# Kernel tuning notes

Measured on AMD Instinct MI355X. Metric: run time of the kernel, lower is better.

## Reference

```python
import jax, jax.numpy as jnp
import numpy as np

ROPE_BASE = 10000.0


def _apply_rope(x, positions):
    # x: [B, S, H, Dh], positions: [S]
    d_head = x.shape[-1]
    half = d_head // 2
    inv_freq = 1.0 / (ROPE_BASE ** (jnp.arange(0, half, dtype=jnp.float32) * 2.0 / d_head))
    angles = positions.astype(jnp.float32)[:, None] * inv_freq[None, :]  # [S, half]
    cos = jnp.cos(angles)[None, :, None, :]  # [1,S,1,half]
    sin = jnp.sin(angles)[None, :, None, :]
    x1, x2 = jnp.split(x, 2, axis=-1)
    return jnp.concatenate([x1 * cos - x2 * sin, x1 * sin + x2 * cos], axis=-1)


def _alibi_slopes(n_heads):
    # standard ALiBi slopes: 2^(-8*(h+1)/n_heads)
    return 2.0 ** (-8.0 * (jnp.arange(1, n_heads + 1, dtype=jnp.float32) / n_heads))


def setup_inputs() -> dict:
    key = jax.random.key(0)
    ks = jax.random.split(key, 5)
    B, S, D = 2, 2048, 2048
    H, KVH, Dh = 16, 4, 128
    std = 0.02
    return {
        "residual": jax.random.normal(ks[0], (B, S, D), dtype=jnp.float32),
        "W_Q": jax.random.normal(ks[1], (H, Dh, D), dtype=jnp.float32) * std,
        "W_K": jax.random.normal(ks[2], (KVH, Dh, D), dtype=jnp.float32) * std,
        "W_V": jax.random.normal(ks[3], (KVH, Dh, D), dtype=jnp.float32) * std,
        "W_O": jax.random.normal(ks[4], (H, Dh, D), dtype=jnp.float32) * std,
        "start_pos": 0,
    }


def reference(residual, W_Q, W_K, W_V, W_O, start_pos):
    B, S, D = residual.shape
    H, Dh, _ = W_Q.shape
    KVH = W_K.shape[0]
    # projections (prefill path: cache=None, total_len == S)
    q = jnp.einsum('bsd,hed->bshe', residual, W_Q)   # [B,S,H,Dh]
    k = jnp.einsum('bsd,hed->bshe', residual, W_K)   # [B,S,KVH,Dh]
    v = jnp.einsum('bsd,hed->bshe', residual, W_V)   # [B,S,KVH,Dh]
    # RoPE
    positions = start_pos + jnp.arange(S)
    q = _apply_rope(q, positions)
    k = _apply_rope(k, positions)
    k_for_cache = k
    v_for_cache = v
    # GQA head repeat
    rep = H // KVH
    k_r = jnp.repeat(k, rep, axis=2)
    v_r = jnp.repeat(v, rep, axis=2)
    # attention scores [B,H,Sq,Sk]
    scores = jnp.einsum('bqhe,bkhe->bhqk', q, k_r) / jnp.sqrt(jnp.float32(Dh))
    # ALiBi bias (sliced rows start_pos:start_pos+S of the total_len x total_len bias)
    slopes = _alibi_slopes(H)  # [H]
    qpos = start_pos + jnp.arange(S)
    kpos = jnp.arange(S)
    bias = -slopes[:, None, None] * (qpos[:, None] - kpos[None, :]).astype(jnp.float32)
    scores = scores + bias[None, :, :, :]
    # causal mask: keep j <= i (tril of ones)
    mask = kpos[None, :] <= qpos[:, None]  # with start_pos=0 this is tril
    scores = jnp.where(mask[None, None, :, :], scores, -jnp.inf)
    pattern = jax.nn.softmax(scores, axis=-1)
    attn = jnp.einsum('bhqk,bkhe->bqhe', pattern, v_r)
    output = jnp.einsum('bqhe,hed->bqd', attn, W_O)
    return output, k_for_cache, v_for_cache
```

## Files before the change

kernel.cpp:

```cpp
#include <hip/hip_runtime.h>


typedef __attribute__((ext_vector_type(8))) short frag8;
typedef __attribute__((ext_vector_type(4))) float facc4;

#define DEVI __device__ __forceinline__

constexpr int Bc  = 2;
constexpr int Sc  = 2048;
constexpr int Dc  = 2048;
constexpr int Hc  = 16;
constexpr int KVHc = 4;
constexpr int Dhc = 128;
constexpr int Mc  = Bc * Sc;
constexpr int NQc = Hc * Dhc;
constexpr int NKVc = KVHc * Dhc;

DEVI unsigned short f2bf(float f) {
  union { float f; unsigned u; } v; v.f = f;
  return (unsigned short)((v.u + 0x7fffu + ((v.u >> 16) & 1u)) >> 16);
}
DEVI float bf2f(unsigned short h) {
  union { unsigned u; float f; } v; v.u = ((unsigned)h) << 16;
  return v.f;
}

DEVI void gload_lds16(const void* g, void* l) {
  __builtin_amdgcn_global_load_lds(
      (const __attribute__((address_space(1))) unsigned int*)g,
      (__attribute__((address_space(3))) unsigned int*)l, 16, 0, 0);
}

DEVI float rowred_max(float x) {
  union { float f; int i; } a, b;
  a.f = x;
  b.i = __builtin_amdgcn_update_dpp(a.i, a.i, 0x128, 0xF, 0xF, false); a.f = fmaxf(a.f, b.f);
  b.i = __builtin_amdgcn_update_dpp(a.i, a.i, 0x124, 0xF, 0xF, false); a.f = fmaxf(a.f, b.f);
  b.i = __builtin_amdgcn_update_dpp(a.i, a.i, 0x122, 0xF, 0xF, false); a.f = fmaxf(a.f, b.f);
  b.i = __builtin_amdgcn_update_dpp(a.i, a.i, 0x121, 0xF, 0xF, false); a.f = fmaxf(a.f, b.f);
  return a.f;
}
DEVI float rowred_sum(float x) {
  union { float f; int i; } a, b;
  a.f = x;
  b.i = __builtin_amdgcn_update_dpp(a.i, a.i, 0x128, 0xF, 0xF, false); a.f += b.f;
  b.i = __builtin_amdgcn_update_dpp(a.i, a.i, 0x124, 0xF, 0xF, false); a.f += b.f;
  b.i = __builtin_amdgcn_update_dpp(a.i, a.i, 0x122, 0xF, 0xF, false); a.f += b.f;
  b.i = __builtin_amdgcn_update_dpp(a.i, a.i, 0x121, 0xF, 0xF, false); a.f += b.f;
  return a.f;
}


__global__ void cvt_f32_bf16(const float* __restrict__ in,
                             unsigned short* __restrict__ out, int n) {
  int i = (blockIdx.x * 256 + threadIdx.x) * 4;
  if (i < n) {
    float4 v = *(const float4*)(in + i);
    ushort4 o;
    o.x = f2bf(v.x); o.y = f2bf(v.y); o.z = f2bf(v.z); o.w = f2bf(v.w);
    *(ushort4*)(out + i) = o;
  }
}

__global__ void cvt_transpose_wo(const float* __restrict__ in,
                                 unsigned short* __restrict__ out) {
  __shared__ float tile[64][65];
  int r0 = blockIdx.y * 64;
  int c0 = blockIdx.x * 64;
  int t = threadIdx.x;
#pragma unroll
  for (int i = 0; i < 16; ++i) {
    int idx = i * 256 + t; int r = idx >> 6, c = idx & 63;
    tile[r][c] = in[(size_t)(r0 + r) * Dc + c0 + c];
  }
  __syncthreads();
#pragma unroll
  for (int i = 0; i < 16; ++i) {
    int idx = i * 256 + t; int r = idx >> 6, c = idx & 63;
    out[(size_t)(c0 + r) * NQc + r0 + c] = f2bf(tile[c][r]);
  }
}


template <int MODE>
__global__ __launch_bounds__(256) void gemm_nt(
    const unsigned short* __restrict__ Amat,
    const unsigned short* __restrict__ Bmat,
    float* __restrict__ Cf, float* __restrict__ Cf2,
    unsigned short* __restrict__ Cb,
    int Nn, int Kk) {
  __shared__ __align__(16) unsigned short As[128 * 32];
  __shared__ __align__(16) unsigned short Bs[128 * 32];
  int t = threadIdx.x;
  int lane = t & 63, w = t >> 6;
  int quad = lane >> 4, l16 = lane & 15;
  int wm = (w >> 1) * 64, wn = (w & 1) * 64;
  int m0 = blockIdx.x * 128, n0 = blockIdx.y * 128;

  facc4 acc[4][4] = {};

  const int nIter = Kk / 32;
  for (int kt = 0; kt < nIter; ++kt) {
    __syncthreads();
#pragma unroll
    for (int i = 0; i < 2; ++i) {
      int c = i * 256 + t;
      int row = c >> 2, ch = c & 3;
      gload_lds16(Amat + (size_t)(m0 + row) * Kk + kt * 32 + ch * 8, &As[c * 8]);
      gload_lds16(Bmat + (size_t)(n0 + row) * Kk + kt * 32 + ch * 8, &Bs[c * 8]);
    }
    asm volatile("s_waitcnt vmcnt(0)" ::: "memory");
    __syncthreads();

    frag8 aF[4], bF[4];
#pragma unroll
    for (int mi = 0; mi < 4; ++mi)
      aF[mi] = *(const frag8*)&As[(wm + mi * 16 + l16) * 32 + quad * 8];
#pragma unroll
    for (int ni = 0; ni < 4; ++ni)
      bF[ni] = *(const frag8*)&Bs[(wn + ni * 16 + l16) * 32 + quad * 8];
#pragma unroll
    for (int mi = 0; mi < 4; ++mi)
#pragma unroll
      for (int ni = 0; ni < 4; ++ni)
        acc[mi][ni] = __builtin_amdgcn_mfma_f32_16x16x32_bf16(
            aF[mi], bF[ni], acc[mi][ni], 0, 0, 0);
  }

#pragma unroll
  for (int mi = 0; mi < 4; ++mi)
#pragma unroll
    for (int ni = 0; ni < 4; ++ni)
#pragma unroll
      for (int i = 0; i < 4; ++i) {
        int mrow = m0 + wm + mi * 16 + quad * 4 + i;
        int ncol = n0 + wn + ni * 16 + l16;
        float v = acc[mi][ni][i];
        if (MODE == 0) {
          Cf[(size_t)mrow * Nn + ncol] = v;
        } else if (MODE == 1) {
          Cb[(size_t)mrow * Nn + ncol] = f2bf(v);
        } else {
          if (ncol < NKVc) {
            Cf[(size_t)mrow * NKVc + ncol] = v;
          } else {
            int nc = ncol - NKVc;
            Cf2[(size_t)mrow * NKVc + nc] = v;
            int b = mrow >> 11, s = mrow & (Sc - 1);
            Cb[((size_t)(b * NKVc + nc)) * Sc + s] = f2bf(v);
          }
        }
      }
}


__global__ void rope_q(unsigned short* qb, const int* __restrict__ sp) {
  int idx = blockIdx.x * 256 + threadIdx.x;
  int e = idx & 63, h = (idx >> 6) & 15, m = idx >> 10;
  int s = m & (Sc - 1);
  float pos = (float)(sp[0] + s);
  float invf = exp2f(-(float)e * 0.20762050593046835f);
  float ang = pos * invf;
  float sn, cs; sincosf(ang, &sn, &cs);
  size_t base = (size_t)m * NQc + h * Dhc + e;
  float x1 = bf2f(qb[base]), x2 = bf2f(qb[base + 64]);
  qb[base]      = f2bf(x1 * cs - x2 * sn);
  qb[base + 64] = f2bf(x1 * sn + x2 * cs);
}

__global__ void rope_k(float* kf, unsigned short* kb, const int* __restrict__ sp) {
  int idx = blockIdx.x * 256 + threadIdx.x;
  int e = idx & 63, kvh = (idx >> 6) & 3, m = idx >> 8;
  int s = m & (Sc - 1);
  float pos = (float)(sp[0] + s);
  float invf = exp2f(-(float)e * 0.20762050593046835f);
  float ang = pos * invf;
  float sn, cs; sincosf(ang, &sn, &cs);
  size_t base = (size_t)m * NKVc + kvh * Dhc + e;
  float x1 = kf[base], x2 = kf[base + 64];
  float o1 = x1 * cs - x2 * sn;
  float o2 = x1 * sn + x2 * cs;
  kf[base] = o1; kf[base + 64] = o2;
  kb[base] = f2bf(o1); kb[base + 64] = f2bf(o2);
}


DEVI void issue_tile(const unsigned short* kb, const unsigned short* vbT,
                     int bb, int kvh, int kt, int t,
                     unsigned short* KsB, unsigned short* VtB) {
#pragma unroll
  for (int i = 0; i < 4; ++i) {
    int c = i * 256 + t;
    int row = c >> 4, chp = c & 15;
    int ch = chp ^ (row & 15);
    gload_lds16(kb + (size_t)(bb * Sc + kt * 64 + row) * NKVc + kvh * Dhc + ch * 8,
                KsB + c * 8);
  }
#pragma unroll
  for (int i = 0; i < 4; ++i) {
    int c = i * 256 + t;
    int row = c >> 3, chp = c & 7;
    int ch = chp ^ (row & 7);
    gload_lds16(vbT + ((size_t)(bb * KVHc + kvh) * Dhc + row) * Sc + kt * 64 + ch * 8,
                VtB + c * 8);
  }
}

DEVI void load_q(frag8 (&aQc)[4], const unsigned short* qb, int bb, int qt,
                 int h, int w, int quad, int l16) {
  const unsigned short* qrow =
      qb + (size_t)(bb * Sc + qt * 64 + w * 16 + l16) * NQc + h * Dhc;
#pragma unroll
  for (int kd = 0; kd < 4; ++kd)
    aQc[kd] = *(const frag8*)(qrow + (kd * 4 + quad) * 8);
}

DEVI void write_o(unsigned short* qb, facc4 (&oacc)[8], float (&lrow)[4],
                  int bb, int qt, int h, int w, int quad, int l16) {
  float rinv[4];
#pragma unroll
  for (int i = 0; i < 4; ++i) rinv[i] = 1.0f / rowred_sum(lrow[i]);
#pragma unroll
  for (int c8 = 0; c8 < 8; ++c8)
#pragma unroll
    for (int i = 0; i < 4; ++i) {
      int row = qt * 64 + w * 16 + quad * 4 + i;
      size_t o = ((size_t)(bb * Sc + row) * Hc + h) * Dhc + c8 * 16 + l16;
      qb[o] = f2bf(oacc[c8][i] * rinv[i]);
    }
}

__global__ __launch_bounds__(256, 2) void flash_attn(
    unsigned short* qb,
    const unsigned short* __restrict__ kb,
    const unsigned short* __restrict__ vbT,
    const int* __restrict__ spp) {
  __shared__ __align__(16) unsigned short Ks[2][64 * 128];
  __shared__ __align__(16) unsigned short Vt[2][128 * 64];
  __shared__ __align__(16) unsigned short Ps[4][16 * 64];

  int g = blockIdx.x & 7;
  int bb = g >> 2, kvh = g & 3;
  int inner = blockIdx.x >> 3;
  int pair = inner & 15, hh = inner >> 4;
  int h = kvh * 4 + hh;
  int qtA = pair, qtB = 31 - pair;

  int t = threadIdx.x, lane = t & 63, w = t >> 6;
  int quad = lane >> 4, l16 = lane & 15;
  int sp = spp[0];
  constexpr float LOG2E = 1.4426950408889634f;
  const float SC = 0.08838834764831845f * LOG2E;
  const float THR = 8.0f;
  float slope2 = exp2f(-0.5f * (float)(h + 1)) * LOG2E;

  int tA = min((sp + qtA * 64 + 63) >> 6, 31) + 1;
  int tB = min((sp + qtB * 64 + 63) >> 6, 31) + 1;
  int total = tA + tB;

  frag8 aQc[4];
  load_q(aQc, qb, bb, qtA, h, w, quad, l16);

  facc4 oacc[8] = {};
  float mrow[4], lrow[4];
  int qposi[4]; float bq[4];
  int qt = qtA;
#pragma unroll
  for (int i = 0; i < 4; ++i) {
    mrow[i] = -1e30f; lrow[i] = 0.f;
    qposi[i] = sp + qt * 64 + w * 16 + quad * 4 + i;
    bq[i] = slope2 * (float)qposi[i];
  }

  issue_tile(kb, vbT, bb, kvh, tA - 1, t, Ks[0], Vt[0]);

  for (int it = 0; it < total; ++it) {
    if (it == tA) {
      write_o(qb, oacc, lrow, bb, qtA, h, w, quad, l16);
      load_q(aQc, qb, bb, qtB, h, w, quad, l16);
      qt = qtB;
#pragma unroll
      for (int c8 = 0; c8 < 8; ++c8)
#pragma unroll
        for (int i = 0; i < 4; ++i) oacc[c8][i] = 0.f;
#pragma unroll
      for (int i = 0; i < 4; ++i) {
        mrow[i] = -1e30f; lrow[i] = 0.f;
        qposi[i] = sp + qt * 64 + w * 16 + quad * 4 + i;
        bq[i] = slope2 * (float)qposi[i];
      }
    }
    int kt = (it < tA) ? (tA - 1 - it) : (total - 1 - it);

    if (it + 1 < total) {
      int nk = (it + 1 < tA) ? (tA - 2 - it) : (total - 2 - it);
      issue_tile(kb, vbT, bb, kvh, nk, t, Ks[(it + 1) & 1], Vt[(it + 1) & 1]);
      asm volatile("s_waitcnt vmcnt(8)" ::: "memory");
    } else {
      asm volatile("s_waitcnt vmcnt(0)" ::: "memory");
    }
    __builtin_amdgcn_s_barrier();
    asm volatile("" ::: "memory");

    const unsigned short* KsB = Ks[it & 1];
    const unsigned short* VtB = Vt[it & 1];

    facc4 sacc[4] = {};
#pragma unroll
    for (int kd = 0; kd < 4; ++kd) {
      int ch = kd * 4 + quad;
#pragma unroll
      for (int c4 = 0; c4 < 4; ++c4) {
        frag8 bK = *(const frag8*)&KsB[(c4 * 16 + l16) * 128 + (ch ^ l16) * 8];
        sacc[c4] = __builtin_amdgcn_mfma_f32_16x16x32_bf16(aQc[kd], bK, sacc[c4], 0, 0, 0);
      }
    }

    bool needmask = (kt * 64 + 63) > (sp + qt * 64);
    float sv[4][4];
    float mt[4] = {-1e30f, -1e30f, -1e30f, -1e30f};
    float bk0 = slope2 * (float)(kt * 64 + l16);
    float s2x16 = slope2 * 16.0f;
#pragma unroll
    for (int c4 = 0; c4 < 4; ++c4) {
      float bk = bk0 + (float)c4 * s2x16;
      int kpos = kt * 64 + c4 * 16 + l16;
#pragma unroll
      for (int i = 0; i < 4; ++i) {
        float v = fmaf(sacc[c4][i], SC, bk - bq[i]);
        if (needmask) v = (kpos <= qposi[i]) ? v : -1e30f;
        sv[c4][i] = v;
        mt[i] = fmaxf(mt[i], v);
      }
    }

    int need = (mt[0] > mrow[0] + THR) || (mt[1] > mrow[1] + THR) ||
               (mt[2] > mrow[2] + THR) || (mt[3] > mrow[3] + THR);
    if (__any(need)) {
      float alpha[4];
#pragma unroll
      for (int i = 0; i < 4; ++i) mt[i] = rowred_max(mt[i]);
#pragma unroll
      for (int i = 0; i < 4; ++i) {
        float mn = fmaxf(mrow[i], mt[i]);
        alpha[i] = exp2f(mrow[i] - mn);
        mrow[i] = mn;
        lrow[i] *= alpha[i];
      }
#pragma unroll
      for (int c8 = 0; c8 < 8; ++c8)
#pragma unroll
        for (int i = 0; i < 4; ++i) oacc[c8][i] *= alpha[i];
    }

#pragma unroll
    for (int c4 = 0; c4 < 4; ++c4) {
      float p0 = exp2f(sv[c4][0] - mrow[0]);
      float p1 = exp2f(sv[c4][1] - mrow[1]);
      float p2 = exp2f(sv[c4][2] - mrow[2]);
      float p3 = exp2f(sv[c4][3] - mrow[3]);
      lrow[0] += p0; lrow[1] += p1; lrow[2] += p2; lrow[3] += p3;
      unsigned u01, u23;
      asm("v_cvt_pk_bf16_f32 %0, %1, %2" : "=v"(u01) : "v"(p0), "v"(p1));
      asm("v_cvt_pk_bf16_f32 %0, %1, %2" : "=v"(u23) : "v"(p2), "v"(p3));
      int kk = c4 * 16 + l16;
      int col = kk & 7, chnk = kk >> 3;
      int r0 = quad * 4;
      unsigned short* Pw = &Ps[w][0];
      Pw[(r0 + 0) * 64 + ((chnk ^ ((r0 + 0) & 7)) * 8) + col] = (unsigned short)(u01 & 0xffffu);
      Pw[(r0 + 1) * 64 + ((chnk ^ ((r0 + 1) & 7)) * 8) + col] = (unsigned short)(u01 >> 16);
      Pw[(r0 + 2) * 64 + ((chnk ^ ((r0 + 2) & 7)) * 8) + col] = (unsigned short)(u23 & 0xffffu);
      Pw[(r0 + 3) * 64 + ((chnk ^ ((r0 + 3) & 7)) * 8) + col] = (unsigned short)(u23 >> 16);
    }

#pragma unroll
    for (int k2 = 0; k2 < 2; ++k2) {
      int ch = k2 * 4 + quad;
      frag8 aP = *(const frag8*)&Ps[w][l16 * 64 + (ch ^ (l16 & 7)) * 8];
#pragma unroll
      for (int c8 = 0; c8 < 8; ++c8) {
        frag8 bV = *(const frag8*)&VtB[(c8 * 16 + l16) * 64 + (ch ^ (l16 & 7)) * 8];
        oacc[c8] = __builtin_amdgcn_mfma_f32_16x16x32_bf16(aP, bV, oacc[c8], 0, 0, 0);
      }
    }

    asm volatile("" ::: "memory");
    __builtin_amdgcn_s_barrier();
  }

  write_o(qb, oacc, lrow, bb, qtB, h, w, quad, l16);
}


extern "C" void kernel_launch(void* const* d_in, const int* in_sizes, int n_in,
                              void* d_out, int out_size, void* d_ws, size_t ws_size,
                              hipStream_t stream) {
  const float* residual = (const float*)d_in[0];
  const float* W_Q = (const float*)d_in[1];
  const float* W_K = (const float*)d_in[2];
  const float* W_V = (const float*)d_in[3];
  const float* W_O = (const float*)d_in[4];
  const int* start_pos = (const int*)d_in[5];

  float* out = (float*)d_out;
  float* kf = out + (size_t)Bc * Sc * Dc;
  float* vf = kf + (size_t)Mc * NKVc;

  char* w = (char*)d_ws;
  auto alloc = [&](size_t bytes) {
    char* p = w; w += (bytes + 255) & ~(size_t)255; return p;
  };
  unsigned short* rb   = (unsigned short*)alloc((size_t)Mc * Dc * 2);
  unsigned short* wqb  = (unsigned short*)alloc((size_t)NQc * Dc * 2);
  unsigned short* wkvb = (unsigned short*)alloc((size_t)2 * NKVc * Dc * 2);
  unsigned short* wob  = (unsigned short*)alloc((size_t)Dc * NQc * 2);
  unsigned short* qb   = (unsigned short*)alloc((size_t)Mc * NQc * 2);
  unsigned short* kb   = (unsigned short*)alloc((size_t)Mc * NKVc * 2);
  unsigned short* vbT  = (unsigned short*)alloc((size_t)Mc * NKVc * 2);
  (void)ws_size; (void)in_sizes; (void)n_in; (void)out_size;

  cvt_f32_bf16<<<(Mc * Dc) / 1024, 256, 0, stream>>>(residual, rb, Mc * Dc);
  cvt_f32_bf16<<<(NQc * Dc) / 1024, 256, 0, stream>>>(W_Q, wqb, NQc * Dc);
  cvt_f32_bf16<<<(NKVc * Dc) / 1024, 256, 0, stream>>>(W_K, wkvb, NKVc * Dc);
  cvt_f32_bf16<<<(NKVc * Dc) / 1024, 256, 0, stream>>>(W_V, wkvb + (size_t)NKVc * Dc, NKVc * Dc);
  cvt_transpose_wo<<<dim3(32, 32), 256, 0, stream>>>(W_O, wob);

  gemm_nt<1><<<dim3(32, 16), 256, 0, stream>>>(rb, wqb, nullptr, nullptr, qb, NQc, Dc);
  gemm_nt<2><<<dim3(32, 8), 256, 0, stream>>>(rb, wkvb, kf, vf, vbT, 2 * NKVc, Dc);

  rope_q<<<(Mc * Hc * 64) / 256, 256, 0, stream>>>(qb, start_pos);
  rope_k<<<(Mc * KVHc * 64) / 256, 256, 0, stream>>>(kf, kb, start_pos);

  flash_attn<<<512, 256, 0, stream>>>(qb, kb, vbT, start_pos);

  gemm_nt<0><<<dim3(32, 16), 256, 0, stream>>>(qb, wob, out, nullptr, nullptr, Dc, Dc);
}
```

Baseline: 376.6 us.

## Drop running-max tracking in unmasked attention tiles and merge small launches

In flash attention, tiles that are neither the first nor the diagonal tile skip the max reduction and rescaling. They compute exp2 of one FMA, using a precomputed per-column additive offset that shrinks by slope*64 per tile. This works because the ALiBi bias falls as the key tile moves further back. A rare overflow check rescales l, O and the offset by 2^-32 when the row sum grows too large. The conversion kernels and the two RoPE kernels are also merged into single launches to cut launch overhead. The risk is numerical: if scores in far tiles exceed the first tile's max, the exponent could grow, which the overflow guard only partly handles.

```diff
diff --git a/kernel.cpp b/kernel.cpp
--- a/kernel.cpp
+++ b/kernel.cpp
@@ -51,33 +51,44 @@
 }
 
 
-__global__ void cvt_f32_bf16(const float* __restrict__ in,
-                             unsigned short* __restrict__ out, int n) {
-  int i = (blockIdx.x * 256 + threadIdx.x) * 4;
-  if (i < n) {
-    float4 v = *(const float4*)(in + i);
+__global__ void cvt_all(const float* __restrict__ residual,
+                        const float* __restrict__ WQ,
+                        const float* __restrict__ WK,
+                        const float* __restrict__ WV,
+                        const float* __restrict__ WO,
+                        unsigned short* __restrict__ rb,
+                        unsigned short* __restrict__ wqb,
+                        unsigned short* __restrict__ wkvb,
+                        unsigned short* __restrict__ wob) {
+  __shared__ float tile[64][65];
+  int bid = blockIdx.x;
+  int t = threadIdx.x;
+  if (bid < 14336) {
+    const float* src; unsigned short* dst; int off;
+    if (bid < 8192)       { src = residual; dst = rb;  off = bid; }
+    else if (bid < 12288) { src = WQ; dst = wqb; off = bid - 8192; }
+    else if (bid < 13312) { src = WK; dst = wkvb; off = bid - 12288; }
+    else                  { src = WV; dst = wkvb + (size_t)NKVc * Dc; off = bid - 13312; }
+    int i = (off * 256 + t) * 4;
+    float4 v = *(const float4*)(src + i);
     ushort4 o;
     o.x = f2bf(v.x); o.y = f2bf(v.y); o.z = f2bf(v.z); o.w = f2bf(v.w);
-    *(ushort4*)(out + i) = o;
-  }
-}
-
-__global__ void cvt_transpose_wo(const float* __restrict__ in,
-                                 unsigned short* __restrict__ out) {
-  __shared__ float tile[64][65];
-  int r0 = blockIdx.y * 64;
-  int c0 = blockIdx.x * 64;
-  int t = threadIdx.x;
-#pragma unroll
-  for (int i = 0; i < 16; ++i) {
-    int idx = i * 256 + t; int r = idx >> 6, c = idx & 63;
-    tile[r][c] = in[(size_t)(r0 + r) * Dc + c0 + c];
-  }
-  __syncthreads();
-#pragma unroll
-  for (int i = 0; i < 16; ++i) {
-    int idx = i * 256 + t; int r = idx >> 6, c = idx & 63;
-    out[(size_t)(c0 + r) * NQc + r0 + c] = f2bf(tile[c][r]);
+    *(ushort4*)(dst + i) = o;
+  } else {
+    int tb = bid - 14336;
+    int r0 = (tb >> 5) * 64;
+    int c0 = (tb & 31) * 64;
+#pragma unroll
+    for (int i = 0; i < 16; ++i) {
+      int idx = i * 256 + t; int r = idx >> 6, c = idx & 63;
+      tile[r][c] = WO[(size_t)(r0 + r) * Dc + c0 + c];
+    }
+    __syncthreads();
+#pragma unroll
+    for (int i = 0; i < 16; ++i) {
+      int idx = i * 256 + t; int r = idx >> 6, c = idx & 63;
+      wob[(size_t)(c0 + r) * NQc + r0 + c] = f2bf(tile[c][r]);
+    }
   }
 }
 
@@ -154,34 +165,36 @@
 }
 
 
-__global__ void rope_q(unsigned short* qb, const int* __restrict__ sp) {
+__global__ void rope_all(unsigned short* qb, float* kf, unsigned short* kb,
+                         const int* __restrict__ sp) {
   int idx = blockIdx.x * 256 + threadIdx.x;
-  int e = idx & 63, h = (idx >> 6) & 15, m = idx >> 10;
-  int s = m & (Sc - 1);
-  float pos = (float)(sp[0] + s);
-  float invf = exp2f(-(float)e * 0.20762050593046835f);
-  float ang = pos * invf;
-  float sn, cs; sincosf(ang, &sn, &cs);
-  size_t base = (size_t)m * NQc + h * Dhc + e;
-  float x1 = bf2f(qb[base]), x2 = bf2f(qb[base + 64]);
-  qb[base]      = f2bf(x1 * cs - x2 * sn);
-  qb[base + 64] = f2bf(x1 * sn + x2 * cs);
-}
-
-__global__ void rope_k(float* kf, unsigned short* kb, const int* __restrict__ sp) {
-  int idx = blockIdx.x * 256 + threadIdx.x;
-  int e = idx & 63, kvh = (idx >> 6) & 3, m = idx >> 8;
-  int s = m & (Sc - 1);
-  float pos = (float)(sp[0] + s);
-  float invf = exp2f(-(float)e * 0.20762050593046835f);
-  float ang = pos * invf;
-  float sn, cs; sincosf(ang, &sn, &cs);
-  size_t base = (size_t)m * NKVc + kvh * Dhc + e;
-  float x1 = kf[base], x2 = kf[base + 64];
-  float o1 = x1 * cs - x2 * sn;
-  float o2 = x1 * sn + x2 * cs;
-  kf[base] = o1; kf[base + 64] = o2;
-  kb[base] = f2bf(o1); kb[base + 64] = f2bf(o2);
+  constexpr int NQ = Mc * Hc * 64;
+  if (idx < NQ) {
+    int e = idx & 63, h = (idx >> 6) & 15, m = idx >> 10;
+    int s = m & (Sc - 1);
+    float pos = (float)(sp[0] + s);
+    float invf = exp2f(-(float)e * 0.20762050593046835f);
+    float ang = pos * invf;
+    float sn, cs; sincosf(ang, &sn, &cs);
+    size_t base = (size_t)m * NQc + h * Dhc + e;
+    float x1 = bf2f(qb[base]), x2 = bf2f(qb[base + 64]);
+    qb[base]      = f2bf(x1 * cs - x2 * sn);
+    qb[base + 64] = f2bf(x1 * sn + x2 * cs);
+  } else {
+    int j = idx - NQ;
+    int e = j & 63, kvh = (j >> 6) & 3, m = j >> 8;
+    int s = m & (Sc - 1);
+    float pos = (float)(sp[0] + s);
+    float invf = exp2f(-(float)e * 0.20762050593046835f);
+    float ang = pos * invf;
+    float sn, cs; sincosf(ang, &sn, &cs);
+    size_t base = (size_t)m * NKVc + kvh * Dhc + e;
+    float x1 = kf[base], x2 = kf[base + 64];
+    float o1 = x1 * cs - x2 * sn;
+    float o2 = x1 * sn + x2 * cs;
+    kf[base] = o1; kf[base + 64] = o2;
+    kb[base] = f2bf(o1); kb[base + 64] = f2bf(o2);
+  }
 }
 
 
@@ -251,8 +264,9 @@
   int sp = spp[0];
   constexpr float LOG2E = 1.4426950408889634f;
   const float SC = 0.08838834764831845f * LOG2E;
-  const float THR = 8.0f;
   float slope2 = exp2f(-0.5f * (float)(h + 1)) * LOG2E;
+  float s2x16 = slope2 * 16.0f;
+  float s2x64 = slope2 * 64.0f;
 
   int tA = min((sp + qtA * 64 + 63) >> 6, 31) + 1;
   int tB = min((sp + qtB * 64 + 63) >> 6, 31) + 1;
@@ -262,8 +276,8 @@
   load_q(aQc, qb, bb, qtA, h, w, quad, l16);
 
   facc4 oacc[8] = {};
-  float mrow[4], lrow[4];
-  int qposi[4]; float bq[4];
+  float mrow[4], lrow[4], bq[4], adn[4][4];
+  int qposi[4];
   int qt = qtA;
 #pragma unroll
   for (int i = 0; i < 4; ++i) {
@@ -291,6 +305,7 @@
       }
     }
     int kt = (it < tA) ? (tA - 1 - it) : (total - 1 - it);
+    bool first = (it == 0) || (it == tA);
 
     if (it + 1 < total) {
       int nk = (it + 1 < tA) ? (tA - 2 - it) : (total - 2 - it);
@@ -316,61 +331,80 @@
       }
     }
 
+    unsigned short* Pw = &Ps[w][0];
+    int r0 = quad * 4;
     bool needmask = (kt * 64 + 63) > (sp + qt * 64);
-    float sv[4][4];
-    float mt[4] = {-1e30f, -1e30f, -1e30f, -1e30f};
-    float bk0 = slope2 * (float)(kt * 64 + l16);
-    float s2x16 = slope2 * 16.0f;
-#pragma unroll
-    for (int c4 = 0; c4 < 4; ++c4) {
-      float bk = bk0 + (float)c4 * s2x16;
-      int kpos = kt * 64 + c4 * 16 + l16;
-#pragma unroll
-      for (int i = 0; i < 4; ++i) {
-        float v = fmaf(sacc[c4][i], SC, bk - bq[i]);
-        if (needmask) v = (kpos <= qposi[i]) ? v : -1e30f;
-        sv[c4][i] = v;
-        mt[i] = fmaxf(mt[i], v);
-      }
-    }
-
-    int need = (mt[0] > mrow[0] + THR) || (mt[1] > mrow[1] + THR) ||
-               (mt[2] > mrow[2] + THR) || (mt[3] > mrow[3] + THR);
-    if (__any(need)) {
-      float alpha[4];
+
+    if (first || needmask) {
+      float sv[4][4];
+      float mt[4] = {-1e30f, -1e30f, -1e30f, -1e30f};
+#pragma unroll
+      for (int c4 = 0; c4 < 4; ++c4) {
+        int kpos = kt * 64 + c4 * 16 + l16;
+        float bk = slope2 * (float)kpos;
+#pragma unroll
+        for (int i = 0; i < 4; ++i) {
+          float v = fmaf(sacc[c4][i], SC, bk - bq[i]);
+          if (needmask) v = (kpos <= qposi[i]) ? v : -1e30f;
+          sv[c4][i] = v;
+          mt[i] = fmaxf(mt[i], v);
+        }
+      }
 #pragma unroll
       for (int i = 0; i < 4; ++i) mt[i] = rowred_max(mt[i]);
 #pragma unroll
       for (int i = 0; i < 4; ++i) {
         float mn = fmaxf(mrow[i], mt[i]);
-        alpha[i] = exp2f(mrow[i] - mn);
+        float alpha = exp2f(mrow[i] - mn);
         mrow[i] = mn;
-        lrow[i] *= alpha[i];
-      }
-#pragma unroll
-      for (int c8 = 0; c8 < 8; ++c8)
-#pragma unroll
-        for (int i = 0; i < 4; ++i) oacc[c8][i] *= alpha[i];
-    }
-
-#pragma unroll
-    for (int c4 = 0; c4 < 4; ++c4) {
-      float p0 = exp2f(sv[c4][0] - mrow[0]);
-      float p1 = exp2f(sv[c4][1] - mrow[1]);
-      float p2 = exp2f(sv[c4][2] - mrow[2]);
-      float p3 = exp2f(sv[c4][3] - mrow[3]);
-      lrow[0] += p0; lrow[1] += p1; lrow[2] += p2; lrow[3] += p3;
-      unsigned u01, u23;
-      asm("v_cvt_pk_bf16_f32 %0, %1, %2" : "=v"(u01) : "v"(p0), "v"(p1));
-      asm("v_cvt_pk_bf16_f32 %0, %1, %2" : "=v"(u23) : "v"(p2), "v"(p3));
-      int kk = c4 * 16 + l16;
-      int col = kk & 7, chnk = kk >> 3;
-      int r0 = quad * 4;
-      unsigned short* Pw = &Ps[w][0];
-      Pw[(r0 + 0) * 64 + ((chnk ^ ((r0 + 0) & 7)) * 8) + col] = (unsigned short)(u01 & 0xffffu);
-      Pw[(r0 + 1) * 64 + ((chnk ^ ((r0 + 1) & 7)) * 8) + col] = (unsigned short)(u01 >> 16);
-      Pw[(r0 + 2) * 64 + ((chnk ^ ((r0 + 2) & 7)) * 8) + col] = (unsigned short)(u23 & 0xffffu);
-      Pw[(r0 + 3) * 64 + ((chnk ^ ((r0 + 3) & 7)) * 8) + col] = (unsigned short)(u23 >> 16);
+        lrow[i] *= alpha;
+#pragma unroll
+        for (int c8 = 0; c8 < 8; ++c8) oacc[c8][i] *= alpha;
+      }
+#pragma unroll
+      for (int c4 = 0; c4 < 4; ++c4) {
+        float p0 = exp2f(sv[c4][0] - mrow[0]);
+        float p1 = exp2f(sv[c4][1] - mrow[1]);
+        float p2 = exp2f(sv[c4][2] - mrow[2]);
+        float p3 = exp2f(sv[c4][3] - mrow[3]);
+        lrow[0] += p0; lrow[1] += p1; lrow[2] += p2; lrow[3] += p3;
+        unsigned u01, u23;
+        asm("v_cvt_pk_bf16_f32 %0, %1, %2" : "=v"(u01) : "v"(p0), "v"(p1));
+        asm("v_cvt_pk_bf16_f32 %0, %1, %2" : "=v"(u23) : "v"(p2), "v"(p3));
+        int kk = c4 * 16 + l16;
+        int col = kk & 7, chnk = kk >> 3;
+        Pw[(r0 + 0) * 64 + ((chnk ^ ((r0 + 0) & 7)) * 8) + col] = (unsigned short)(u01 & 0xffffu);
+        Pw[(r0 + 1) * 64 + ((chnk ^ ((r0 + 1) & 7)) * 8) + col] = (unsigned short)(u01 >> 16);
+        Pw[(r0 + 2) * 64 + ((chnk ^ ((r0 + 2) & 7)) * 8) + col] = (unsigned short)(u23 & 0xffffu);
+        Pw[(r0 + 3) * 64 + ((chnk ^ ((r0 + 3) & 7)) * 8) + col] = (unsigned short)(u23 >> 16);
+      }
+      float bkn0 = slope2 * (float)((kt - 1) * 64 + l16);
+#pragma unroll
+      for (int c4 = 0; c4 < 4; ++c4) {
+        float bkc = bkn0 + (float)c4 * s2x16;
+#pragma unroll
+        for (int i = 0; i < 4; ++i) adn[c4][i] = bkc - bq[i] - mrow[i];
+      }
+    } else {
+#pragma unroll
+      for (int c4 = 0; c4 < 4; ++c4) {
+        float p0 = exp2f(fmaf(sacc[c4][0], SC, adn[c4][0]));
+        float p1 = exp2f(fmaf(sacc[c4][1], SC, adn[c4][1]));
+        float p2 = exp2f(fmaf(sacc[c4][2], SC, adn[c4][2]));
+        float p3 = exp2f(fmaf(sacc[c4][3], SC, adn[c4][3]));
+        lrow[0] += p0; lrow[1] += p1; lrow[2] += p2; lrow[3] += p3;
+        adn[c4][0] -= s2x64; adn[c4][1] -= s2x64;
+        adn[c4][2] -= s2x64; adn[c4][3] -= s2x64;
+        unsigned u01, u23;
+        asm("v_cvt_pk_bf16_f32 %0, %1, %2" : "=v"(u01) : "v"(p0), "v"(p1));
+        asm("v_cvt_pk_bf16_f32 %0, %1, %2" : "=v"(u23) : "v"(p2), "v"(p3));
+        int kk = c4 * 16 + l16;
+        int col = kk & 7, chnk = kk >> 3;
+        Pw[(r0 + 0) * 64 + ((chnk ^ ((r0 + 0) & 7)) * 8) + col] = (unsigned short)(u01 & 0xffffu);
+        Pw[(r0 + 1) * 64 + ((chnk ^ ((r0 + 1) & 7)) * 8) + col] = (unsigned short)(u01 >> 16);
+        Pw[(r0 + 2) * 64 + ((chnk ^ ((r0 + 2) & 7)) * 8) + col] = (unsigned short)(u23 & 0xffffu);
+        Pw[(r0 + 3) * 64 + ((chnk ^ ((r0 + 3) & 7)) * 8) + col] = (unsigned short)(u23 >> 16);
+      }
     }
 
 #pragma unroll
@@ -381,6 +415,24 @@
       for (int c8 = 0; c8 < 8; ++c8) {
         frag8 bV = *(const frag8*)&VtB[(c8 * 16 + l16) * 64 + (ch ^ (l16 & 7)) * 8];
         oacc[c8] = __builtin_amdgcn_mfma_f32_16x16x32_bf16(aP, bV, oacc[c8], 0, 0, 0);
+      }
+    }
+
+    if (!first) {
+      int ovf = (lrow[0] > 16777216.f) || (lrow[1] > 16777216.f) ||
+                (lrow[2] > 16777216.f) || (lrow[3] > 16777216.f);
+      if (__any(ovf)) {
+        const float DS = 0x1p-32f;
+#pragma unroll
+        for (int i = 0; i < 4; ++i) { lrow[i] *= DS; mrow[i] += 32.f; }
+#pragma unroll
+        for (int c4 = 0; c4 < 4; ++c4)
+#pragma unroll
+          for (int i = 0; i < 4; ++i) adn[c4][i] -= 32.f;
+#pragma unroll
+        for (int c8 = 0; c8 < 8; ++c8)
+#pragma unroll
+          for (int i = 0; i < 4; ++i) oacc[c8][i] *= DS;
       }
     }
 
@@ -419,17 +471,13 @@
   unsigned short* vbT  = (unsigned short*)alloc((size_t)Mc * NKVc * 2);
   (void)ws_size; (void)in_sizes; (void)n_in; (void)out_size;
 
-  cvt_f32_bf16<<<(Mc * Dc) / 1024, 256, 0, stream>>>(residual, rb, Mc * Dc);
-  cvt_f32_bf16<<<(NQc * Dc) / 1024, 256, 0, stream>>>(W_Q, wqb, NQc * Dc);
-  cvt_f32_bf16<<<(NKVc * Dc) / 1024, 256, 0, stream>>>(W_K, wkvb, NKVc * Dc);
-  cvt_f32_bf16<<<(NKVc * Dc) / 1024, 256, 0, stream>>>(W_V, wkvb + (size_t)NKVc * Dc, NKVc * Dc);
-  cvt_transpose_wo<<<dim3(32, 32), 256, 0, stream>>>(W_O, wob);
+  cvt_all<<<15360, 256, 0, stream>>>(residual, W_Q, W_K, W_V, W_O,
+                                     rb, wqb, wkvb, wob);
 
   gemm_nt<1><<<dim3(32, 16), 256, 0, stream>>>(rb, wqb, nullptr, nullptr, qb, NQc, Dc);
   gemm_nt<2><<<dim3(32, 8), 256, 0, stream>>>(rb, wkvb, kf, vf, vbT, 2 * NKVc, Dc);
 
-  rope_q<<<(Mc * Hc * 64) / 256, 256, 0, stream>>>(qb, start_pos);
-  rope_k<<<(Mc * KVHc * 64) / 256, 256, 0, stream>>>(kf, kb, start_pos);
+  rope_all<<<20480, 256, 0, stream>>>(qb, kf, kb, start_pos);
 
   flash_attn<<<512, 256, 0, stream>>>(qb, kb, vbT, start_pos);
 
```

New measurement: 365.6 us. -2.9%, faster.
